# Performance work log

Measured on AMD Instinct MI355X. Metric: run time of the kernel, lower is better.

The kernel has to match this reference:

```python
import jax, jax.numpy as jnp
import numpy as np

N_NODES = 100000
N_EDGES = 1600000
IN_FEATS = 64
H_FEATS = 64
NUM_CLASSES = 16


def gcn_conv(x, edge_index, edge_weight, W, b, n_nodes):
    # Linear transform first (PyG GCNConv)
    x = x @ W  # [N, F_out]
    row = edge_index[0]
    col = edge_index[1]
    # Add self-loops with weight 1
    loop = jnp.arange(n_nodes, dtype=row.dtype)
    row = jnp.concatenate([row, loop])
    col = jnp.concatenate([col, loop])
    ew = jnp.concatenate([edge_weight, jnp.ones((n_nodes,), dtype=edge_weight.dtype)])
    # Symmetric normalization: deg accumulated at target (col)
    deg = jax.ops.segment_sum(ew, col, num_segments=n_nodes)
    dinv = jnp.where(deg > 0, jax.lax.rsqrt(deg), 0.0)
    norm = dinv[row] * ew * dinv[col]  # [E+N]
    # Gather source features, weight, scatter-add to targets
    msg = x[row] * norm[:, None]  # [E+N, F_out]
    out = jax.ops.segment_sum(msg, col, num_segments=n_nodes)
    return out + b


def setup_inputs() -> dict:
    key = jax.random.key(0)
    ks = jax.random.split(key, 7)
    in_feat = jax.random.normal(ks[0], (N_NODES, IN_FEATS), dtype=jnp.float32)
    edge_index = jax.random.randint(ks[1], (2, N_EDGES), 0, N_NODES, dtype=jnp.int64)
    edge_weight = jax.random.uniform(ks[2], (N_EDGES,), dtype=jnp.float32)
    W1 = jax.random.normal(ks[3], (IN_FEATS, H_FEATS), dtype=jnp.float32) / np.sqrt(IN_FEATS)
    b1 = jnp.zeros((H_FEATS,), dtype=jnp.float32)
    W2 = jax.random.normal(ks[4], (H_FEATS, NUM_CLASSES), dtype=jnp.float32) / np.sqrt(H_FEATS)
    b2 = jnp.zeros((NUM_CLASSES,), dtype=jnp.float32)
    return {"in_feat": in_feat, "edge_index": edge_index, "edge_weight": edge_weight,
            "W1": W1, "b1": b1, "W2": W2, "b2": b2}


def reference(in_feat, edge_index, edge_weight, W1, b1, W2, b2):
    n = in_feat.shape[0]
    h = gcn_conv(in_feat, edge_index, edge_weight, W1, b1, n)
    h = jax.nn.relu(h)
    h = gcn_conv(h, edge_index, edge_weight, W2, b2, n)
    return h
```

## Files before the change

### kernel.cpp

```cpp
#include <hip/hip_runtime.h>


struct __align__(8) Edge { int r; float w; };

#define XPAD 68

__device__ __forceinline__ unsigned short f2bf(float f) {
  unsigned u = __float_as_uint(f);
  u = (u + 0x7FFFu + ((u >> 16) & 1u)) >> 16;
  return (unsigned short)u;
}
__device__ __forceinline__ float bf2f(unsigned short h) {
  return __uint_as_float(((unsigned)h) << 16);
}

__global__ __launch_bounds__(256) void zero_cnt(int* cnt, int N) {
  int i = blockIdx.x * 256 + threadIdx.x;
  if (i < N) cnt[i] = 0;
}

__global__ __launch_bounds__(256) void rank_kernel(const int* __restrict__ col,
    int* cnt, int* __restrict__ rank, int E) {
  int e = blockIdx.x * 256 + threadIdx.x;
  if (e < E) rank[e] = atomicAdd(&cnt[col[e]], 1);
}

__global__ __launch_bounds__(1024) void scan_kernel(const int* __restrict__ cnt,
    int* __restrict__ indptr, int N) {
  __shared__ int wsum[16];
  int tid = threadIdx.x;
  int lane = tid & 63, wid = tid >> 6;
  int carry = 0;
  for (int base = 0; base < N; base += 4096) {
    int i0 = base + tid * 4;
    int v0 = (i0 + 0 < N) ? cnt[i0 + 0] : 0;
    int v1 = (i0 + 1 < N) ? cnt[i0 + 1] : 0;
    int v2 = (i0 + 2 < N) ? cnt[i0 + 2] : 0;
    int v3 = (i0 + 3 < N) ? cnt[i0 + 3] : 0;
    int s = v0 + v1 + v2 + v3;
    int x = s;
    #pragma unroll
    for (int d = 1; d < 64; d <<= 1) { int y = __shfl_up(x, d); if (lane >= d) x += y; }
    if (lane == 63) wsum[wid] = x;
    __syncthreads();
    if (wid == 0 && lane < 16) {
      int t = wsum[lane];
      #pragma unroll
      for (int d = 1; d < 16; d <<= 1) { int y = __shfl_up(t, d); if (lane >= d) t += y; }
      wsum[lane] = t;
    }
    __syncthreads();
    int waveoff = (wid == 0) ? 0 : wsum[wid - 1];
    int b0 = carry + waveoff + (x - s);
    if (i0 + 0 < N) indptr[i0 + 0] = b0;
    if (i0 + 1 < N) indptr[i0 + 1] = b0 + v0;
    if (i0 + 2 < N) indptr[i0 + 2] = b0 + v0 + v1;
    if (i0 + 3 < N) indptr[i0 + 3] = b0 + v0 + v1 + v2;
    int total = wsum[15];
    __syncthreads();
    carry += total;
  }
  if (tid == 0) indptr[N] = carry;
}

__global__ __launch_bounds__(256) void fill_kernel(const int* __restrict__ row,
    const int* __restrict__ col, const float* __restrict__ ew,
    const int* __restrict__ rank, const int* __restrict__ indptr,
    Edge* __restrict__ edges, int E) {
  int e = blockIdx.x * 256 + threadIdx.x;
  if (e < E) {
    int c = col[e];
    Edge ed; ed.r = row[e]; ed.w = ew[e];
    edges[indptr[c] + rank[e]] = ed;
  }
}

__global__ __launch_bounds__(256) void dinv_kernel(const Edge* __restrict__ edges,
    const int* __restrict__ indptr, float* __restrict__ dinv, int N) {
  int tid = threadIdx.x;
  int lane = tid & 63;
  int sub = lane >> 4, j = lane & 15;
  int node = blockIdx.x * 16 + (tid >> 6) * 4 + sub;
  bool valid = node < N;
  int s = 0, e = 0;
  if (valid) { s = indptr[node]; e = indptr[node + 1]; }
  float sum = 0.f;
  for (int b = s; b < e; b += 16) {
    int m = min(16, e - b);
    if (j < m) sum += edges[b + j].w;
  }
  #pragma unroll
  for (int d = 1; d < 16; d <<= 1) sum += __shfl_xor(sum, d, 16);
  if (valid && j == 0) dinv[node] = 1.0f / sqrtf(1.0f + sum);
}

__global__ __launch_bounds__(256) void norm_kernel(Edge* edges,
    const float* __restrict__ dinv, int E) {
  int i = blockIdx.x * 256 + threadIdx.x;
  if (i < E) {
    Edge e = edges[i];
    e.w *= dinv[e.r];
    edges[i] = e;
  }
}

__global__ __launch_bounds__(256) void gemm64t(const float* __restrict__ X,
    const float* __restrict__ W, unsigned short* __restrict__ Yb, int N) {
  __shared__ float Xs[64 * XPAD];
  __shared__ float Ws[64 * 64];
  int tid = threadIdx.x;
  int nb = blockIdx.x * 64;
  {
    const float4* Wv = (const float4*)W;
    float4* Wsv = (float4*)Ws;
    #pragma unroll
    for (int p = 0; p < 4; ++p) Wsv[p * 256 + tid] = Wv[p * 256 + tid];
  }
  #pragma unroll
  for (int p = 0; p < 4; ++p) {
    int g = p * 256 + tid;
    int r = g >> 4, c4 = g & 15;
    int node = nb + r;
    float4 v = make_float4(0.f, 0.f, 0.f, 0.f);
    if (node < N) v = *(const float4*)&X[(size_t)node * 64 + c4 * 4];
    *(float4*)&Xs[r * XPAD + c4 * 4] = v;
  }
  __syncthreads();
  int jg = tid & 15;
  int ng = tid >> 4;
  float acc[4][4] = {};
  for (int k = 0; k < 64; k += 4) {
    float4 xv[4], wv[4];
    #pragma unroll
    for (int i = 0; i < 4; ++i) xv[i] = *(const float4*)&Xs[(ng * 4 + i) * XPAD + k];
    #pragma unroll
    for (int kk = 0; kk < 4; ++kk) wv[kk] = *(const float4*)&Ws[(k + kk) * 64 + jg * 4];
    #pragma unroll
    for (int i = 0; i < 4; ++i) {
      #pragma unroll
      for (int kk = 0; kk < 4; ++kk) {
        float xs = ((const float*)&xv[i])[kk];
        acc[i][0] = fmaf(xs, ((const float*)&wv[kk])[0], acc[i][0]);
        acc[i][1] = fmaf(xs, ((const float*)&wv[kk])[1], acc[i][1]);
        acc[i][2] = fmaf(xs, ((const float*)&wv[kk])[2], acc[i][2]);
        acc[i][3] = fmaf(xs, ((const float*)&wv[kk])[3], acc[i][3]);
      }
    }
  }
  #pragma unroll
  for (int i = 0; i < 4; ++i) {
    int node = nb + ng * 4 + i;
    if (node < N) {
      ushort4 o;
      o.x = f2bf(acc[i][0]); o.y = f2bf(acc[i][1]);
      o.z = f2bf(acc[i][2]); o.w = f2bf(acc[i][3]);
      *(ushort4*)&Yb[(size_t)node * 64 + jg * 4] = o;
    }
  }
}

__global__ __launch_bounds__(256) void gemm16t(const float* __restrict__ Xh,
    const float* __restrict__ W2, float* __restrict__ Y, int N) {
  __shared__ float Xs[64 * XPAD];
  __shared__ float Ws[64 * 16];
  int tid = threadIdx.x;
  int nb = blockIdx.x * 64;
  ((float4*)Ws)[tid] = ((const float4*)W2)[tid];
  #pragma unroll
  for (int p = 0; p < 4; ++p) {
    int g = p * 256 + tid;
    int r = g >> 4, c4 = g & 15;
    int node = nb + r;
    float4 v = make_float4(0.f, 0.f, 0.f, 0.f);
    if (node < N) v = *(const float4*)&Xh[(size_t)node * 64 + c4 * 4];
    *(float4*)&Xs[r * XPAD + c4 * 4] = v;
  }
  __syncthreads();
  int node_l = tid >> 2;
  int jg = tid & 3;
  float acc[4] = {};
  for (int k = 0; k < 64; k += 4) {
    float4 xv = *(const float4*)&Xs[node_l * XPAD + k];
    #pragma unroll
    for (int kk = 0; kk < 4; ++kk) {
      float4 wv = *(const float4*)&Ws[(k + kk) * 16 + jg * 4];
      float xs = ((const float*)&xv)[kk];
      acc[0] = fmaf(xs, wv.x, acc[0]);
      acc[1] = fmaf(xs, wv.y, acc[1]);
      acc[2] = fmaf(xs, wv.z, acc[2]);
      acc[3] = fmaf(xs, wv.w, acc[3]);
    }
  }
  int node = nb + node_l;
  if (node < N)
    *(float4*)&Y[(size_t)node * 16 + jg * 4] = make_float4(acc[0], acc[1], acc[2], acc[3]);
}

__global__ __launch_bounds__(256) void agg64(const unsigned short* __restrict__ h1b,
    const int* __restrict__ indptr, const Edge* __restrict__ edges,
    const float* __restrict__ dinv, const float* __restrict__ b1,
    float* __restrict__ hout, int N) {
  __shared__ Edge eds[4][64];
  int tid = threadIdx.x;
  int lane = tid & 63;
  int wid = tid >> 6;
  int node = blockIdx.x * 4 + wid;
  if (node >= N) return;
  int s = indptr[node], eend = indptr[node + 1];
  float di = dinv[node];
  float self = di * bf2f(h1b[(size_t)node * 64 + lane]);
  float acc = 0.f, accB = 0.f;
  for (int base = s; base < eend; base += 64) {
    int m = min(64, eend - base);
    if (lane < m) eds[wid][lane] = edges[base + lane];
    int t = 0;
    for (; t + 1 < m; t += 2) {
      Edge e0 = eds[wid][t];
      Edge e1 = eds[wid][t + 1];
      acc  = fmaf(e0.w, bf2f(h1b[(size_t)e0.r * 64 + lane]), acc);
      accB = fmaf(e1.w, bf2f(h1b[(size_t)e1.r * 64 + lane]), accB);
    }
    if (t < m) {
      Edge e0 = eds[wid][t];
      acc = fmaf(e0.w, bf2f(h1b[(size_t)e0.r * 64 + lane]), acc);
    }
  }
  float res = fmaf(di, acc + accB + self, b1[lane]);
  hout[(size_t)node * 64 + lane] = fmaxf(res, 0.f);
}

__global__ __launch_bounds__(256) void agg16(const float* __restrict__ h2,
    const int* __restrict__ indptr, const Edge* __restrict__ edges,
    const float* __restrict__ dinv, const float* __restrict__ b2,
    float* __restrict__ out, int N) {
  __shared__ Edge eds[4][4][17];
  int tid = threadIdx.x;
  int lane = tid & 63;
  int wid = tid >> 6;
  int sub = lane >> 4, j = lane & 15;
  int node = blockIdx.x * 16 + wid * 4 + sub;
  bool valid = node < N;
  int s = 0, eend = 0;
  float di = 0.f, self = 0.f;
  if (valid) {
    s = indptr[node]; eend = indptr[node + 1];
    di = dinv[node];
    self = di * h2[(size_t)node * 16 + j];
  }
  float acc = 0.f, accB = 0.f;
  for (int base = s; base < eend; base += 16) {
    int m = min(16, eend - base);
    if (j < m) eds[wid][sub][j] = edges[base + j];
    int t = 0;
    for (; t + 1 < m; t += 2) {
      Edge e0 = eds[wid][sub][t];
      Edge e1 = eds[wid][sub][t + 1];
      acc  = fmaf(e0.w, h2[(size_t)e0.r * 16 + j], acc);
      accB = fmaf(e1.w, h2[(size_t)e1.r * 16 + j], accB);
    }
    if (t < m) {
      Edge e0 = eds[wid][sub][t];
      acc = fmaf(e0.w, h2[(size_t)e0.r * 16 + j], acc);
    }
  }
  if (valid) out[(size_t)node * 16 + j] = fmaf(di, acc + accB + self, b2[j]);
}

extern "C" void kernel_launch(void* const* d_in, const int* in_sizes, int n_in,
                              void* d_out, int out_size, void* d_ws, size_t ws_size,
                              hipStream_t stream) {
  const float* X   = (const float*)d_in[0];
  const int*   eix = (const int*)d_in[1];
  const float* ew  = (const float*)d_in[2];
  const float* W1  = (const float*)d_in[3];
  const float* b1  = (const float*)d_in[4];
  const float* W2  = (const float*)d_in[5];
  const float* b2  = (const float*)d_in[6];
  float* out = (float*)d_out;

  const int N = in_sizes[0] / 64;
  const int E = in_sizes[1] / 2;
  const int* row = eix;
  const int* col = eix + E;

  char* ws = (char*)d_ws;
  size_t off = 0;
  auto alloc = [&](size_t bytes) -> void* {
    void* p = ws + off;
    off += (bytes + 255) & ~(size_t)255;
    return p;
  };
  int*   cnt    = (int*)  alloc((size_t)N * 4);
  int*   indptr = (int*)  alloc(((size_t)N + 1) * 4);
  int*   rank   = (int*)  alloc((size_t)E * 4);
  Edge*  edges  = (Edge*) alloc((size_t)E * 8);
  float* dinv   = (float*)alloc((size_t)N * 4);
  unsigned short* h1b = (unsigned short*)alloc((size_t)N * 64 * 2);
  float* hrelu  = (float*)alloc((size_t)N * 64 * 4);
  float* h2     = (float*)alloc((size_t)N * 16 * 4);
  if (off > ws_size) return;

  int nbN = (N + 255) / 256;
  int nbE = (E + 255) / 256;
  int nbT = (N + 63) / 64;

  zero_cnt   <<<nbN, 256, 0, stream>>>(cnt, N);
  rank_kernel<<<nbE, 256, 0, stream>>>(col, cnt, rank, E);
  scan_kernel<<<1, 1024, 0, stream>>>(cnt, indptr, N);
  fill_kernel<<<nbE, 256, 0, stream>>>(row, col, ew, rank, indptr, edges, E);
  dinv_kernel<<<(N + 15) / 16, 256, 0, stream>>>(edges, indptr, dinv, N);
  norm_kernel<<<nbE, 256, 0, stream>>>(edges, dinv, E);

  gemm64t<<<nbT, 256, 0, stream>>>(X, W1, h1b, N);
  agg64  <<<(N + 3) / 4, 256, 0, stream>>>(h1b, indptr, edges, dinv, b1, hrelu, N);
  gemm16t<<<nbT, 256, 0, stream>>>(hrelu, W2, h2, N);
  agg16  <<<(N + 15) / 16, 256, 0, stream>>>(h2, indptr, edges, dinv, b2, out, N);
}
```

Baseline: 395.6 us.

## Fold source-side degree normalization into GEMM outputs and prefetch scan inputs

Removes the per-edge norm pass by scaling each node's transformed features by dinv in the GEMM epilogues, so the aggregation kernels only need the raw edge weight and the target-side dinv. The self-loop term now uses the pre-scaled feature directly. The single-block scan also loads the next 4096-element chunk of counts before it scans the current chunk, to hide load latency. The trade-off is a small extra dinv load per GEMM block, and bf16 rounding is now applied after the dinv scaling.

Result: faster. 385.9 us (-2.4%).

```diff
diff --git a/kernel.cpp b/kernel.cpp
--- a/kernel.cpp
+++ b/kernel.cpp
@@ -31,12 +31,21 @@
   int tid = threadIdx.x;
   int lane = tid & 63, wid = tid >> 6;
   int carry = 0;
+  int i0 = tid * 4;
+  int v0 = (i0 + 0 < N) ? cnt[i0 + 0] : 0;
+  int v1 = (i0 + 1 < N) ? cnt[i0 + 1] : 0;
+  int v2 = (i0 + 2 < N) ? cnt[i0 + 2] : 0;
+  int v3 = (i0 + 3 < N) ? cnt[i0 + 3] : 0;
   for (int base = 0; base < N; base += 4096) {
-    int i0 = base + tid * 4;
-    int v0 = (i0 + 0 < N) ? cnt[i0 + 0] : 0;
-    int v1 = (i0 + 1 < N) ? cnt[i0 + 1] : 0;
-    int v2 = (i0 + 2 < N) ? cnt[i0 + 2] : 0;
-    int v3 = (i0 + 3 < N) ? cnt[i0 + 3] : 0;
+    int nbase = base + 4096;
+    int n0 = 0, n1 = 0, n2 = 0, n3 = 0;
+    if (nbase < N) {
+      int j0 = nbase + tid * 4;
+      n0 = (j0 + 0 < N) ? cnt[j0 + 0] : 0;
+      n1 = (j0 + 1 < N) ? cnt[j0 + 1] : 0;
+      n2 = (j0 + 2 < N) ? cnt[j0 + 2] : 0;
+      n3 = (j0 + 3 < N) ? cnt[j0 + 3] : 0;
+    }
     int s = v0 + v1 + v2 + v3;
     int x = s;
     #pragma unroll
@@ -51,14 +60,16 @@
     }
     __syncthreads();
     int waveoff = (wid == 0) ? 0 : wsum[wid - 1];
+    int st = base + tid * 4;
     int b0 = carry + waveoff + (x - s);
-    if (i0 + 0 < N) indptr[i0 + 0] = b0;
-    if (i0 + 1 < N) indptr[i0 + 1] = b0 + v0;
-    if (i0 + 2 < N) indptr[i0 + 2] = b0 + v0 + v1;
-    if (i0 + 3 < N) indptr[i0 + 3] = b0 + v0 + v1 + v2;
+    if (st + 0 < N) indptr[st + 0] = b0;
+    if (st + 1 < N) indptr[st + 1] = b0 + v0;
+    if (st + 2 < N) indptr[st + 2] = b0 + v0 + v1;
+    if (st + 3 < N) indptr[st + 3] = b0 + v0 + v1 + v2;
     int total = wsum[15];
     __syncthreads();
     carry += total;
+    v0 = n0; v1 = n1; v2 = n2; v3 = n3;
   }
   if (tid == 0) indptr[N] = carry;
 }
@@ -94,20 +105,12 @@
   if (valid && j == 0) dinv[node] = 1.0f / sqrtf(1.0f + sum);
 }
 
-__global__ __launch_bounds__(256) void norm_kernel(Edge* edges,
-    const float* __restrict__ dinv, int E) {
-  int i = blockIdx.x * 256 + threadIdx.x;
-  if (i < E) {
-    Edge e = edges[i];
-    e.w *= dinv[e.r];
-    edges[i] = e;
-  }
-}
-
 __global__ __launch_bounds__(256) void gemm64t(const float* __restrict__ X,
-    const float* __restrict__ W, unsigned short* __restrict__ Yb, int N) {
+    const float* __restrict__ W, const float* __restrict__ dinv,
+    unsigned short* __restrict__ Yb, int N) {
   __shared__ float Xs[64 * XPAD];
   __shared__ float Ws[64 * 64];
+  __shared__ float dvs[64];
   int tid = threadIdx.x;
   int nb = blockIdx.x * 64;
   {
@@ -116,6 +119,7 @@
     #pragma unroll
     for (int p = 0; p < 4; ++p) Wsv[p * 256 + tid] = Wv[p * 256 + tid];
   }
+  if (tid < 64) dvs[tid] = (nb + tid < N) ? dinv[nb + tid] : 0.f;
   #pragma unroll
   for (int p = 0; p < 4; ++p) {
     int g = p * 256 + tid;
@@ -151,21 +155,25 @@
   for (int i = 0; i < 4; ++i) {
     int node = nb + ng * 4 + i;
     if (node < N) {
+      float dv = dvs[ng * 4 + i];
       ushort4 o;
-      o.x = f2bf(acc[i][0]); o.y = f2bf(acc[i][1]);
-      o.z = f2bf(acc[i][2]); o.w = f2bf(acc[i][3]);
+      o.x = f2bf(dv * acc[i][0]); o.y = f2bf(dv * acc[i][1]);
+      o.z = f2bf(dv * acc[i][2]); o.w = f2bf(dv * acc[i][3]);
       *(ushort4*)&Yb[(size_t)node * 64 + jg * 4] = o;
     }
   }
 }
 
 __global__ __launch_bounds__(256) void gemm16t(const float* __restrict__ Xh,
-    const float* __restrict__ W2, float* __restrict__ Y, int N) {
+    const float* __restrict__ W2, const float* __restrict__ dinv,
+    float* __restrict__ Y, int N) {
   __shared__ float Xs[64 * XPAD];
   __shared__ float Ws[64 * 16];
+  __shared__ float dvs[64];
   int tid = threadIdx.x;
   int nb = blockIdx.x * 64;
   ((float4*)Ws)[tid] = ((const float4*)W2)[tid];
+  if (tid < 64) dvs[tid] = (nb + tid < N) ? dinv[nb + tid] : 0.f;
   #pragma unroll
   for (int p = 0; p < 4; ++p) {
     int g = p * 256 + tid;
@@ -192,11 +200,14 @@
     }
   }
   int node = nb + node_l;
-  if (node < N)
-    *(float4*)&Y[(size_t)node * 16 + jg * 4] = make_float4(acc[0], acc[1], acc[2], acc[3]);
-}
-
-__global__ __launch_bounds__(256) void agg64(const unsigned short* __restrict__ h1b,
+  if (node < N) {
+    float dv = dvs[node_l];
+    *(float4*)&Y[(size_t)node * 16 + jg * 4] =
+        make_float4(dv * acc[0], dv * acc[1], dv * acc[2], dv * acc[3]);
+  }
+}
+
+__global__ __launch_bounds__(256) void agg64(const unsigned short* __restrict__ g1b,
     const int* __restrict__ indptr, const Edge* __restrict__ edges,
     const float* __restrict__ dinv, const float* __restrict__ b1,
     float* __restrict__ hout, int N) {
@@ -208,7 +219,7 @@
   if (node >= N) return;
   int s = indptr[node], eend = indptr[node + 1];
   float di = dinv[node];
-  float self = di * bf2f(h1b[(size_t)node * 64 + lane]);
+  float selfv = bf2f(g1b[(size_t)node * 64 + lane]);
   float acc = 0.f, accB = 0.f;
   for (int base = s; base < eend; base += 64) {
     int m = min(64, eend - base);
@@ -217,19 +228,19 @@
     for (; t + 1 < m; t += 2) {
       Edge e0 = eds[wid][t];
       Edge e1 = eds[wid][t + 1];
-      acc  = fmaf(e0.w, bf2f(h1b[(size_t)e0.r * 64 + lane]), acc);
-      accB = fmaf(e1.w, bf2f(h1b[(size_t)e1.r * 64 + lane]), accB);
+      acc  = fmaf(e0.w, bf2f(g1b[(size_t)e0.r * 64 + lane]), acc);
+      accB = fmaf(e1.w, bf2f(g1b[(size_t)e1.r * 64 + lane]), accB);
     }
     if (t < m) {
       Edge e0 = eds[wid][t];
-      acc = fmaf(e0.w, bf2f(h1b[(size_t)e0.r * 64 + lane]), acc);
-    }
-  }
-  float res = fmaf(di, acc + accB + self, b1[lane]);
+      acc = fmaf(e0.w, bf2f(g1b[(size_t)e0.r * 64 + lane]), acc);
+    }
+  }
+  float res = fmaf(di, acc + accB + selfv, b1[lane]);
   hout[(size_t)node * 64 + lane] = fmaxf(res, 0.f);
 }
 
-__global__ __launch_bounds__(256) void agg16(const float* __restrict__ h2,
+__global__ __launch_bounds__(256) void agg16(const float* __restrict__ g2,
     const int* __restrict__ indptr, const Edge* __restrict__ edges,
     const float* __restrict__ dinv, const float* __restrict__ b2,
     float* __restrict__ out, int N) {
@@ -241,11 +252,11 @@
   int node = blockIdx.x * 16 + wid * 4 + sub;
   bool valid = node < N;
   int s = 0, eend = 0;
-  float di = 0.f, self = 0.f;
+  float di = 0.f, selfv = 0.f;
   if (valid) {
     s = indptr[node]; eend = indptr[node + 1];
     di = dinv[node];
-    self = di * h2[(size_t)node * 16 + j];
+    selfv = g2[(size_t)node * 16 + j];
   }
   float acc = 0.f, accB = 0.f;
   for (int base = s; base < eend; base += 16) {
@@ -255,15 +266,15 @@
     for (; t + 1 < m; t += 2) {
       Edge e0 = eds[wid][sub][t];
       Edge e1 = eds[wid][sub][t + 1];
-      acc  = fmaf(e0.w, h2[(size_t)e0.r * 16 + j], acc);
-      accB = fmaf(e1.w, h2[(size_t)e1.r * 16 + j], accB);
+      acc  = fmaf(e0.w, g2[(size_t)e0.r * 16 + j], acc);
+      accB = fmaf(e1.w, g2[(size_t)e1.r * 16 + j], accB);
     }
     if (t < m) {
       Edge e0 = eds[wid][sub][t];
-      acc = fmaf(e0.w, h2[(size_t)e0.r * 16 + j], acc);
-    }
-  }
-  if (valid) out[(size_t)node * 16 + j] = fmaf(di, acc + accB + self, b2[j]);
+      acc = fmaf(e0.w, g2[(size_t)e0.r * 16 + j], acc);
+    }
+  }
+  if (valid) out[(size_t)node * 16 + j] = fmaf(di, acc + accB + selfv, b2[j]);
 }
 
 extern "C" void kernel_launch(void* const* d_in, const int* in_sizes, int n_in,
@@ -295,9 +306,9 @@
   int*   rank   = (int*)  alloc((size_t)E * 4);
   Edge*  edges  = (Edge*) alloc((size_t)E * 8);
   float* dinv   = (float*)alloc((size_t)N * 4);
-  unsigned short* h1b = (unsigned short*)alloc((size_t)N * 64 * 2);
+  unsigned short* g1b = (unsigned short*)alloc((size_t)N * 64 * 2);
   float* hrelu  = (float*)alloc((size_t)N * 64 * 4);
-  float* h2     = (float*)alloc((size_t)N * 16 * 4);
+  float* g2     = (float*)alloc((size_t)N * 16 * 4);
   if (off > ws_size) return;
 
   int nbN = (N + 255) / 256;
@@ -309,10 +320,9 @@
   scan_kernel<<<1, 1024, 0, stream>>>(cnt, indptr, N);
   fill_kernel<<<nbE, 256, 0, stream>>>(row, col, ew, rank, indptr, edges, E);
   dinv_kernel<<<(N + 15) / 16, 256, 0, stream>>>(edges, indptr, dinv, N);
-  norm_kernel<<<nbE, 256, 0, stream>>>(edges, dinv, E);
-
-  gemm64t<<<nbT, 256, 0, stream>>>(X, W1, h1b, N);
-  agg64  <<<(N + 3) / 4, 256, 0, stream>>>(h1b, indptr, edges, dinv, b1, hrelu, N);
-  gemm16t<<<nbT, 256, 0, stream>>>(hrelu, W2, h2, N);
-  agg16  <<<(N + 15) / 16, 256, 0, stream>>>(h2, indptr, edges, dinv, b2, out, N);
-}
+
+  gemm64t<<<nbT, 256, 0, stream>>>(X, W1, dinv, g1b, N);
+  agg64  <<<(N + 3) / 4, 256, 0, stream>>>(g1b, indptr, edges, dinv, b1, hrelu, N);
+  gemm16t<<<nbT, 256, 0, stream>>>(hrelu, W2, dinv, g2, N);
+  agg16  <<<(N + 15) / 16, 256, 0, stream>>>(g2, indptr, edges, dinv, b2, out, N);
+}
```
